# Performance work log

Hardware: AMD Instinct MI355X
Metric: run time of the kernel (lower is better)

Reference implementation:

```python
import jax, jax.numpy as jnp
import numpy as np
import math

H = 16          # attn_heads
DK = 64         # features_dec // attn_heads
NEG = -1e9      # additive causal mask value
EPS = 1e-6      # LayerNorm eps (annotated transformer)


def get_slopes(n):
    def p2(m):
        start = 2.0 ** (-(2.0 ** (-(math.log2(m) - 3))))
        return [start * start ** i for i in range(m)]
    if math.log2(n).is_integer():
        return p2(n)
    cp = 2 ** math.floor(math.log2(n))
    return p2(cp) + get_slopes(2 * cp)[0::2][: n - cp]


def setup_inputs() -> dict:
    key = jax.random.key(0)
    ks = jax.random.split(key, 12)
    B, S, FT, FDZ, FDEC, FD = 8, 1024, 16, 768, 1024, 16

    def lin(k, out_d, in_d):
        return jax.random.normal(k, (out_d, in_d), jnp.float32) / np.float32(np.sqrt(in_d))

    return {
        "z_sample": jax.random.normal(ks[0], (B, FDZ), jnp.float32),
        "r_traj": jax.random.normal(ks[1], (B, S, FT), jnp.float32),
        "dense_w": lin(ks[2], FDEC, FDZ + FT), "dense_b": jnp.zeros((FDEC,), jnp.float32),
        "ln_g": jnp.ones((FDEC,), jnp.float32), "ln_b": jnp.zeros((FDEC,), jnp.float32),
        "wq": lin(ks[3], FDEC, FDEC), "bq": jnp.zeros((FDEC,), jnp.float32),
        "wk": lin(ks[4], FDEC, FDEC), "bk": jnp.zeros((FDEC,), jnp.float32),
        "wv": lin(ks[5], FDEC, FDEC), "bv": jnp.zeros((FDEC,), jnp.float32),
        "wo": lin(ks[6], FDEC, FDEC), "bo": jnp.zeros((FDEC,), jnp.float32),
        "dec_w": lin(ks[7], FD, FDEC), "dec_b": jnp.zeros((FD,), jnp.float32),
    }


def reference(z_sample, r_traj, dense_w, dense_b, ln_g, ln_b,
              wq, bq, wk, bk, wv, bv, wo, bo, dec_w, dec_b):
    B, S, _ = r_traj.shape
    # concat trajectory features with broadcast latent sample -> [B,S,in_size]
    x = jnp.concatenate(
        [r_traj, jnp.broadcast_to(z_sample[:, None, :], (B, S, z_sample.shape[-1]))], axis=-1)
    x = x @ dense_w.T + dense_b  # [B,S,FDEC]

    # causal additive mask + ALiBi bias: bias[h,i,j] = causal(i,j) + slope_h * j
    slopes = jnp.asarray(get_slopes(H), jnp.float32)
    causal = jnp.triu(jnp.full((S, S), NEG, jnp.float32), k=1)
    bias = causal[None, :, :] + slopes[:, None, None] * jnp.arange(S, dtype=jnp.float32)[None, None, :]  # [H,S,S]

    # pre-norm sublayer: x + attn(LN(x))  (dropout=0 / eval)
    mu = x.mean(-1, keepdims=True)
    var = x.var(-1, keepdims=True)
    xn = ln_g * (x - mu) / jnp.sqrt(var + EPS) + ln_b

    def heads(w, b):
        return (xn @ w.T + b).reshape(B, S, H, DK).transpose(0, 2, 1, 3)  # [B,H,S,DK]

    q, k, v = heads(wq, bq), heads(wk, bk), heads(wv, bv)
    scores = jnp.einsum('bhid,bhjd->bhij', q, k) / np.float32(np.sqrt(DK)) + bias[None]
    attn = jax.nn.softmax(scores, axis=-1)
    o = jnp.einsum('bhij,bhjd->bhid', attn, v).transpose(0, 2, 1, 3).reshape(B, S, H * DK)
    x = x + o @ wo.T + bo

    # decode_state then transpose(-2,-1) -> [B, features_d, S]
    return (x @ dec_w.T + dec_b).transpose(0, 2, 1)
```

## Files before the change

kernel.cpp:

```cpp
#include <hip/hip_runtime.h>

static constexpr int Bn   = 8;
static constexpr int S    = 1024;
static constexpr int FT   = 16;
static constexpr int FDZ  = 768;
static constexpr int INK  = 784;
static constexpr int FDEC = 1024;
static constexpr int M    = Bn * S;
static constexpr int H    = 16;
static constexpr int FD   = 16;

typedef __bf16 bf16x8 __attribute__((ext_vector_type(8)));
typedef float  f32x4  __attribute__((ext_vector_type(4)));

__device__ __forceinline__ unsigned short f2b(float f) {
  return __builtin_bit_cast(unsigned short, static_cast<__bf16>(f));
}
__device__ __forceinline__ float b2f(unsigned short u) {
  return (float)__builtin_bit_cast(__bf16, u);
}

__device__ __forceinline__ void gload16(const void* g, void* l) {
  __builtin_amdgcn_global_load_lds(
      (const __attribute__((address_space(1))) unsigned int*)g,
      (__attribute__((address_space(3))) unsigned int*)l, 16, 0, 0);
}

__global__ __launch_bounds__(256) void k_prep(const float* __restrict__ dnw,
                                              const float* __restrict__ wq,
                                              const float* __restrict__ wk,
                                              const float* __restrict__ wv,
                                              const float* __restrict__ dcw,
                                              const float* __restrict__ bq,
                                              const float* __restrict__ bk,
                                              const float* __restrict__ bv,
                                              unsigned short* __restrict__ w3,
                                              unsigned short* __restrict__ dwb,
                                              float* __restrict__ b3,
                                              unsigned short* __restrict__ wt16) {
  const int bid = blockIdx.x, tid = threadIdx.x;
  const int c = tid * 4;
  if (bid < 3072) {
    const int r = bid;
    const float* src = (r < 1024) ? wq : (r < 2048 ? wk : wv);
    const int rr = r & 1023;
    float4 v = *reinterpret_cast<const float4*>(&src[(size_t)rr * 1024 + c]);
    unsigned short o4[4] = {f2b(v.x), f2b(v.y), f2b(v.z), f2b(v.w)};
    *reinterpret_cast<uint2*>(&w3[(size_t)r * 1024 + c]) = *reinterpret_cast<uint2*>(o4);
  } else if (bid < 3088) {
    const int r = bid - 3072;
    float4 v = *reinterpret_cast<const float4*>(&dcw[(size_t)r * 1024 + c]);
    unsigned short o4[4] = {f2b(v.x), f2b(v.y), f2b(v.z), f2b(v.w)};
    *reinterpret_cast<uint2*>(&dwb[(size_t)r * 1024 + c]) = *reinterpret_cast<uint2*>(o4);
  } else if (bid < 3091) {
    const int r = bid - 3088;
    const float* s = (r == 0) ? bq : (r == 1 ? bk : bv);
    *reinterpret_cast<float4*>(&b3[r * 1024 + c]) =
        *reinterpret_cast<const float4*>(&s[c]);
  } else {
    const int idx = (bid - 3091) * 256 + tid;
    const int k = idx >> 10, cc = idx & 1023;
    wt16[k * 1024 + cc] = f2b(dnw[(size_t)cc * INK + k]);
  }
}

__global__ __launch_bounds__(256) void k_wcomb1(const float* __restrict__ dcw,
                                                const float* __restrict__ wo,
                                                const float* __restrict__ bo,
                                                const float* __restrict__ dcb,
                                                float* __restrict__ part,
                                                float* __restrict__ bias2) {
  const int tid = threadIdx.x;
  if (blockIdx.x < 64) {
    const int kb = blockIdx.x;
    const int c = tid * 4;
    const int k0 = kb * 16;
    float4 wv[16];
#pragma unroll
    for (int k = 0; k < 16; k++)
      wv[k] = *reinterpret_cast<const float4*>(&wo[(size_t)(k0 + k) * 1024 + c]);
#pragma unroll
    for (int i = 0; i < 16; i++) {
      float4 a = make_float4(0.f, 0.f, 0.f, 0.f);
#pragma unroll
      for (int k = 0; k < 16; k++) {
        float d = dcw[i * 1024 + k0 + k];
        a.x += d * wv[k].x; a.y += d * wv[k].y;
        a.z += d * wv[k].z; a.w += d * wv[k].w;
      }
      *reinterpret_cast<float4*>(&part[((size_t)kb * 16 + i) * 1024 + c]) = a;
    }
  } else {
    const int lane = tid & 63, w = tid >> 6;
    for (int q = 0; q < 4; q++) {
      int f = w * 4 + q;
      const float* dp = &dcw[(size_t)f * 1024];
      float s = 0.f;
#pragma unroll
      for (int t = 0; t < 16; t++) {
        int k = lane + t * 64;
        s += dp[k] * bo[k];
      }
      for (int off = 32; off; off >>= 1) s += __shfl_down(s, off);
      if (lane == 0) bias2[f] = s + dcb[f];
    }
  }
}

__global__ __launch_bounds__(256) void k_wcomb2(const float* __restrict__ part,
                                                unsigned short* __restrict__ wcombb) {
  const int idx = blockIdx.x * 256 + threadIdx.x;
  float s = 0.f;
#pragma unroll 8
  for (int kb = 0; kb < 64; kb++) s += part[(size_t)kb * 16384 + idx];
  wcombb[idx] = f2b(s);
}

__global__ __launch_bounds__(256) void k_za(const float* __restrict__ z,
                                            const float* __restrict__ dnw,
                                            float* __restrict__ za) {
  const int tid = threadIdx.x, lane = tid & 63, w = tid >> 6;
  const int idx = blockIdx.x * 4 + w;
  const int col = idx >> 3, b = idx & 7;
  const float* wp = &dnw[(size_t)col * INK + FT];
  const float* zp = &z[b * FDZ];
  float s = 0.f;
#pragma unroll
  for (int i = 0; i < 12; i++) {
    int k = lane + i * 64;
    s += wp[k] * zp[k];
  }
  for (int off = 32; off; off >>= 1) s += __shfl_down(s, off);
  if (lane == 0) za[b * 1024 + col] = s;
}

__global__ __launch_bounds__(256) void k_dense_ln(const float* __restrict__ rt,
                                                  const float* __restrict__ za,
                                                  const float* __restrict__ dnb,
                                                  const float* __restrict__ lng,
                                                  const float* __restrict__ lnb,
                                                  const unsigned short* __restrict__ wt16g,
                                                  unsigned short* __restrict__ xres,
                                                  unsigned short* __restrict__ xn) {
  __shared__ unsigned short wt[16 * 1024];
  __shared__ float ss[4], qq[4];
  const int tid = threadIdx.x, lane = tid & 63, wv = tid >> 6;
  const int c0 = tid * 4;
#pragma unroll
  for (int i = 0; i < 8; i++)
    reinterpret_cast<uint4*>(wt)[tid + 256 * i] =
        reinterpret_cast<const uint4*>(wt16g)[tid + 256 * i];
  const float4 bv  = *reinterpret_cast<const float4*>(&dnb[c0]);
  const float4 gv  = *reinterpret_cast<const float4*>(&lng[c0]);
  const float4 bev = *reinterpret_cast<const float4*>(&lnb[c0]);
  __syncthreads();

  for (int r = 0; r < 4; ++r) {
    const int m = blockIdx.x * 4 + r;
    const int b = m >> 10;
    float rtv[16];
    {
      float4 t0 = *reinterpret_cast<const float4*>(&rt[m * 16 + 0]);
      float4 t1 = *reinterpret_cast<const float4*>(&rt[m * 16 + 4]);
      float4 t2 = *reinterpret_cast<const float4*>(&rt[m * 16 + 8]);
      float4 t3 = *reinterpret_cast<const float4*>(&rt[m * 16 + 12]);
      rtv[0]=t0.x; rtv[1]=t0.y; rtv[2]=t0.z; rtv[3]=t0.w;
      rtv[4]=t1.x; rtv[5]=t1.y; rtv[6]=t1.z; rtv[7]=t1.w;
      rtv[8]=t2.x; rtv[9]=t2.y; rtv[10]=t2.z; rtv[11]=t2.w;
      rtv[12]=t3.x; rtv[13]=t3.y; rtv[14]=t3.z; rtv[15]=t3.w;
    }
    float4 zav = *reinterpret_cast<const float4*>(&za[b * 1024 + c0]);
    float acc[4] = {zav.x + bv.x, zav.y + bv.y, zav.z + bv.z, zav.w + bv.w};
#pragma unroll
    for (int k = 0; k < 16; ++k) {
      uint2 wraw = *reinterpret_cast<const uint2*>(&wt[k * 1024 + c0]);
      const unsigned short* wp = reinterpret_cast<const unsigned short*>(&wraw);
      float rk = rtv[k];
      acc[0] += rk * b2f(wp[0]);
      acc[1] += rk * b2f(wp[1]);
      acc[2] += rk * b2f(wp[2]);
      acc[3] += rk * b2f(wp[3]);
    }
    float s = acc[0] + acc[1] + acc[2] + acc[3];
    float q = acc[0]*acc[0] + acc[1]*acc[1] + acc[2]*acc[2] + acc[3]*acc[3];
    for (int off = 32; off; off >>= 1) { s += __shfl_down(s, off); q += __shfl_down(q, off); }
    if (lane == 0) { ss[wv] = s; qq[wv] = q; }
    __syncthreads();
    float St = ss[0] + ss[1] + ss[2] + ss[3];
    float Qt = qq[0] + qq[1] + qq[2] + qq[3];
    float mu  = St * (1.f / 1024.f);
    float var = Qt * (1.f / 1024.f) - mu * mu;
    float rstd = rsqrtf(var + 1e-6f);
    unsigned short xo[4], no[4];
    xo[0] = f2b(acc[0]); no[0] = f2b(gv.x * (acc[0] - mu) * rstd + bev.x);
    xo[1] = f2b(acc[1]); no[1] = f2b(gv.y * (acc[1] - mu) * rstd + bev.y);
    xo[2] = f2b(acc[2]); no[2] = f2b(gv.z * (acc[2] - mu) * rstd + bev.z);
    xo[3] = f2b(acc[3]); no[3] = f2b(gv.w * (acc[3] - mu) * rstd + bev.w);
    *reinterpret_cast<uint2*>(&xres[(size_t)m * 1024 + c0]) = *reinterpret_cast<uint2*>(xo);
    *reinterpret_cast<uint2*>(&xn[(size_t)m * 1024 + c0])   = *reinterpret_cast<uint2*>(no);
    __syncthreads();
  }
}

template<int EPI>
__global__ __launch_bounds__(256, 3) void k_gemm1(const unsigned short* __restrict__ A, int lda,
                                                  const unsigned short* __restrict__ Bw, int ldb,
                                                  int K, int N,
                                                  const float* __restrict__ bias,
                                                  unsigned short* __restrict__ Cb) {
  __shared__ __align__(16) unsigned short As[3 * 128 * 32];
  __shared__ __align__(16) unsigned short Bs[3 * 128 * 32];
  const int tid = threadIdx.x, lane = tid & 63, w = tid >> 6;
  const int wr = w >> 1, wc = w & 1;
  const int lr = lane & 15, lg = lane >> 4;

  const int xcd = blockIdx.x & 7;
  const int j   = blockIdx.x >> 3;
  const int m0  = (xcd * 8 + (j & 7)) * 128;
  const int n0  = (j >> 3) * 128;

  const int nt = K >> 5;

  const int g0 = tid;
  const int r0g = g0 >> 2, c0g = (g0 & 3) ^ ((r0g >> 1) & 3);
  const int g1 = tid + 256;
  const int r1g = g1 >> 2, c1g = (g1 & 3) ^ ((r1g >> 1) & 3);
  const unsigned short* srcA0 = A + (size_t)(m0 + r0g) * lda + c0g * 8;
  const unsigned short* srcA1 = A + (size_t)(m0 + r1g) * lda + c1g * 8;
  const unsigned short* srcB0 = Bw + (size_t)(n0 + r0g) * ldb + c0g * 8;
  const unsigned short* srcB1 = Bw + (size_t)(n0 + r1g) * ldb + c1g * 8;
  const int d0 = (w * 64) * 8;
  const int d1 = (256 + w * 64) * 8;

  int offA[4], offB[4];
#pragma unroll
  for (int mi = 0; mi < 4; mi++) {
    int r = wr * 64 + mi * 16 + lr;
    offA[mi] = r * 32 + (lg ^ ((r >> 1) & 3)) * 8;
  }
#pragma unroll
  for (int ni = 0; ni < 4; ni++) {
    int r = wc * 64 + ni * 16 + lr;
    offB[ni] = r * 32 + (lg ^ ((r >> 1) & 3)) * 8;
  }

  f32x4 acc[4][4];
#pragma unroll
  for (int i = 0; i < 4; i++)
#pragma unroll
    for (int j2 = 0; j2 < 4; j2++)
#pragma unroll
      for (int e = 0; e < 4; e++) acc[i][j2][e] = 0.f;

  auto stage = [&](int tt) {
    const int sl = tt % 3;
    const size_t ko = (size_t)tt * 32;
    gload16(srcA0 + ko, &As[sl * 4096 + d0]);
    gload16(srcA1 + ko, &As[sl * 4096 + d1]);
    gload16(srcB0 + ko, &Bs[sl * 4096 + d0]);
    gload16(srcB1 + ko, &Bs[sl * 4096 + d1]);
  };
  auto compute = [&](int tt) {
    const int sl = (tt % 3) * 4096;
    bf16x8 af[4], bfr[4];
#pragma unroll
    for (int mi = 0; mi < 4; mi++)
      af[mi] = *reinterpret_cast<const bf16x8*>(&As[sl + offA[mi]]);
#pragma unroll
    for (int ni = 0; ni < 4; ni++)
      bfr[ni] = *reinterpret_cast<const bf16x8*>(&Bs[sl + offB[ni]]);
    __builtin_amdgcn_s_setprio(1);
#pragma unroll
    for (int mi = 0; mi < 4; mi++)
#pragma unroll
      for (int ni = 0; ni < 4; ni++)
        acc[mi][ni] = __builtin_amdgcn_mfma_f32_16x16x32_bf16(af[mi], bfr[ni], acc[mi][ni], 0, 0, 0);
    __builtin_amdgcn_s_setprio(0);
  };

  stage(0); stage(1);

  int t = 0;
  for (; t < nt - 2; ++t) {
    asm volatile("s_waitcnt vmcnt(4)" ::: "memory");
    __builtin_amdgcn_s_barrier();
    stage(t + 2);
    compute(t);
  }
  asm volatile("s_waitcnt vmcnt(4)" ::: "memory");
  __builtin_amdgcn_s_barrier();
  compute(t); ++t;
  asm volatile("s_waitcnt vmcnt(0)" ::: "memory");
  __builtin_amdgcn_s_barrier();
  compute(t);

#pragma unroll
  for (int mi = 0; mi < 4; mi++)
#pragma unroll
    for (int ni = 0; ni < 4; ni++) {
      int col = n0 + wc * 64 + ni * 16 + lr;
      float bv = bias ? bias[col] : 0.f;
#pragma unroll
      for (int jj = 0; jj < 4; jj++) {
        int row = m0 + wr * 64 + mi * 16 + lg * 4 + jj;
        float v = acc[mi][ni][jj] + bv;
        Cb[(size_t)row * N + col] = f2b(v);
      }
    }
}

__global__ __launch_bounds__(512, 4) void k_attn(const unsigned short* __restrict__ qkv,
                                                 unsigned short* __restrict__ o) {
  __shared__ unsigned short Ks[2][64][72];
  __shared__ unsigned short Vt[2][64][72];
  __shared__ unsigned short Pl[8][16][72];
  const int tid = threadIdx.x, lane = tid & 63, w = tid >> 6;
  const int bh = blockIdx.x, b = bh >> 4, h = bh & 15;
  const int lr = lane & 15, lg = lane >> 4, lg4 = lg * 4;
  const int krow = tid >> 3, c8 = (tid & 7) << 3;
  const int kb8 = krow >> 3, kl = krow & 7, vq = tid & 7;
  const float slope2 = exp2f(-0.5f * (float)(h + 1)) * 1.44269504f;
  const float sc2 = 0.125f * 1.44269504f;

  for (int ph = 0; ph < 2; ++ph) {
    const int qb = ph ? (7 - (int)blockIdx.y) : (int)blockIdx.y;
    const int q0 = qb * 128;
    const int qlo = q0 + w * 16;
    const int qa = qlo + lr;

    bf16x8 qf0, qf1;
    {
      const unsigned short* qp = &qkv[(size_t)(b * 1024 + qlo + lr) * 3072 + h * 64];
      qf0 = *reinterpret_cast<const bf16x8*>(qp + lg * 8);
      qf1 = *reinterpret_cast<const bf16x8*>(qp + 32 + lg * 8);
    }
    float mrun = -3.0e38f, lrun = 0.f;
    f32x4 accO[4];
    for (int dn = 0; dn < 4; dn++)
      for (int e = 0; e < 4; e++) accO[dn][e] = 0.f;

    const int nt = 2 * qb + 2;
    uint4 kr, vr;
    {
      const size_t base = (size_t)(b * 1024 + krow) * 3072 + h * 64;
      kr = *reinterpret_cast<const uint4*>(&qkv[base + 1024 + c8]);
      vr = *reinterpret_cast<const uint4*>(&qkv[base + 2048 + c8]);
    }
    *reinterpret_cast<uint4*>(&Ks[0][krow][c8]) = kr;
    {
      const unsigned short* vs = reinterpret_cast<const unsigned short*>(&vr);
      for (int jj = 0; jj < 8; jj++)
        Vt[0][c8 + jj][((kb8 ^ vq) << 3) | kl] = vs[jj];
    }
    __syncthreads();

    for (int kt = 0; kt < nt; ++kt) {
      const int kb = kt << 6;
      const int cb = kt & 1, nb = cb ^ 1;
      const bool hn = (kt + 1 < nt);
      if (hn) {
        const size_t base = (size_t)(b * 1024 + kb + 64 + krow) * 3072 + h * 64;
        kr = *reinterpret_cast<const uint4*>(&qkv[base + 1024 + c8]);
        vr = *reinterpret_cast<const uint4*>(&qkv[base + 2048 + c8]);
      }
      const bool act = (kb <= qlo + 15);
      float f = 1.f;
      if (act) {
        f32x4 sf[4];
        for (int kn = 0; kn < 4; kn++) {
          f32x4 zz;
          for (int e = 0; e < 4; e++) zz[e] = 0.f;
          bf16x8 kf0 = *reinterpret_cast<const bf16x8*>(&Ks[cb][kn * 16 + lr][lg * 8]);
          bf16x8 kf1 = *reinterpret_cast<const bf16x8*>(&Ks[cb][kn * 16 + lr][32 + lg * 8]);
          zz = __builtin_amdgcn_mfma_f32_16x16x32_bf16(kf0, qf0, zz, 0, 0, 0);
          zz = __builtin_amdgcn_mfma_f32_16x16x32_bf16(kf1, qf1, zz, 0, 0, 0);
          sf[kn] = zz;
        }
        const bool needmask = (kb + 63 > qlo);
        float sc[4][4];
        float ml = -3.0e38f;
        for (int kn = 0; kn < 4; kn++) {
          float alib = slope2 * (float)(kb + kn * 16 + lg4);
          for (int jj = 0; jj < 4; jj++) {
            float v = fmaf(sf[kn][jj], sc2, alib + slope2 * (float)jj);
            if (needmask && (kb + kn * 16 + lg4 + jj > qa)) v = -3.0e38f;
            sc[kn][jj] = v;
            ml = fmaxf(ml, v);
          }
        }
        ml = fmaxf(ml, __shfl_xor(ml, 16));
        ml = fmaxf(ml, __shfl_xor(ml, 32));
        float mnew = fmaxf(mrun, ml);
        f = exp2f(mrun - mnew);
        float rs = 0.f;
        for (int kn = 0; kn < 4; kn++) {
          __bf16 pb[4];
          for (int jj = 0; jj < 4; jj++) {
            float pv = exp2f(sc[kn][jj] - mnew);
            rs += pv;
            pb[jj] = (__bf16)pv;
          }
          *reinterpret_cast<uint2*>(&Pl[w][lr][kn * 16 + lg4]) =
              *reinterpret_cast<uint2*>(pb);
        }
        rs += __shfl_xor(rs, 16);
        rs += __shfl_xor(rs, 32);
        lrun = lrun * f + rs;
        mrun = mnew;
      }
      if (hn) {
        *reinterpret_cast<uint4*>(&Ks[nb][krow][c8]) = kr;
        const unsigned short* vs = reinterpret_cast<const unsigned short*>(&vr);
        for (int jj = 0; jj < 8; jj++)
          Vt[nb][c8 + jj][((kb8 ^ vq) << 3) | kl] = vs[jj];
      }
      if (act) {
        float fj[4];
        for (int jj = 0; jj < 4; jj++) fj[jj] = __shfl(f, (lane & 48) | (lg4 + jj));
        for (int dn = 0; dn < 4; dn++)
          for (int jj = 0; jj < 4; jj++) accO[dn][jj] *= fj[jj];
        asm volatile("s_waitcnt lgkmcnt(0)" ::: "memory");
        for (int ks = 0; ks < 2; ks++) {
          bf16x8 pa = *reinterpret_cast<const bf16x8*>(&Pl[w][lr][ks * 32 + lg * 8]);
          for (int dn = 0; dn < 4; dn++) {
            int d = dn * 16 + lr;
            bf16x8 vb = *reinterpret_cast<const bf16x8*>(
                &Vt[cb][d][(((ks * 4 + lg) ^ (d >> 3)) << 3)]);
            accO[dn] = __builtin_amdgcn_mfma_f32_16x16x32_bf16(pa, vb, accO[dn], 0, 0, 0);
          }
        }
      }
      __syncthreads();
    }
    float linv[4];
    for (int jj = 0; jj < 4; jj++)
      linv[jj] = 1.f / __shfl(lrun, (lane & 48) | (lg4 + jj));
    for (int dn = 0; dn < 4; dn++)
      for (int jj = 0; jj < 4; jj++) {
        int row = qlo + lg4 + jj;
        int d = dn * 16 + lr;
        o[(size_t)(b * 1024 + row) * 1024 + h * 64 + d] = f2b(accO[dn][jj] * linv[jj]);
      }
  }
}

__global__ __launch_bounds__(256) void k_dec2(const unsigned short* __restrict__ xres,
                                              const unsigned short* __restrict__ ob,
                                              const unsigned short* __restrict__ dwb,
                                              const unsigned short* __restrict__ wcombb,
                                              const float* __restrict__ bias2,
                                              float* __restrict__ out) {
  const int tid = threadIdx.x, lane = tid & 63, w = tid >> 6;
  const int lr = lane & 15, lg = lane >> 4;
  const int sb = blockIdx.x * 4 + w;
  const int r0 = sb * 16;
  f32x4 acc;
  for (int e = 0; e < 4; e++) acc[e] = 0.f;
  const unsigned short* arow1 = &xres[(size_t)(r0 + lr) * 1024];
  const unsigned short* arow2 = &ob[(size_t)(r0 + lr) * 1024];
  const unsigned short* brow1 = &dwb[(size_t)lr * 1024];
  const unsigned short* brow2 = &wcombb[(size_t)lr * 1024];
  for (int k0 = 0; k0 < 1024; k0 += 32) {
    bf16x8 a1 = *reinterpret_cast<const bf16x8*>(arow1 + k0 + lg * 8);
    bf16x8 b1 = *reinterpret_cast<const bf16x8*>(brow1 + k0 + lg * 8);
    acc = __builtin_amdgcn_mfma_f32_16x16x32_bf16(a1, b1, acc, 0, 0, 0);
    bf16x8 a2 = *reinterpret_cast<const bf16x8*>(arow2 + k0 + lg * 8);
    bf16x8 b2 = *reinterpret_cast<const bf16x8*>(brow2 + k0 + lg * 8);
    acc = __builtin_amdgcn_mfma_f32_16x16x32_bf16(a2, b2, acc, 0, 0, 0);
  }
  const int b = r0 >> 10;
  const int sl = (r0 & 1023) + lg * 4;
  float bias = bias2[lr];
  float4 res;
  res.x = acc[0] + bias; res.y = acc[1] + bias; res.z = acc[2] + bias; res.w = acc[3] + bias;
  *reinterpret_cast<float4*>(&out[(size_t)(b * 16 + lr) * 1024 + sl]) = res;
}

extern "C" void kernel_launch(void* const* d_in, const int* in_sizes, int n_in,
                              void* d_out, int out_size, void* d_ws, size_t ws_size,
                              hipStream_t stream) {
  (void)in_sizes; (void)n_in; (void)out_size;
  const float* z   = (const float*)d_in[0];
  const float* rt  = (const float*)d_in[1];
  const float* dnw = (const float*)d_in[2];
  const float* dnb = (const float*)d_in[3];
  const float* lng = (const float*)d_in[4];
  const float* lnb = (const float*)d_in[5];
  const float* wq  = (const float*)d_in[6];
  const float* bq  = (const float*)d_in[7];
  const float* wk  = (const float*)d_in[8];
  const float* bk  = (const float*)d_in[9];
  const float* wv  = (const float*)d_in[10];
  const float* bv  = (const float*)d_in[11];
  const float* wo  = (const float*)d_in[12];
  const float* bo  = (const float*)d_in[13];
  const float* dcw = (const float*)d_in[14];
  const float* dcb = (const float*)d_in[15];
  float* out = (float*)d_out;

  char* p = (char*)d_ws;
  unsigned short* xres  = (unsigned short*)p; p += (size_t)M * FDEC * 2;
  unsigned short* xn    = (unsigned short*)p; p += (size_t)M * FDEC * 2;
  unsigned short* w3    = (unsigned short*)p; p += (size_t)3 * FDEC * FDEC * 2;
  float* b3             = (float*)p;          p += (size_t)3 * FDEC * 4;
  unsigned short* qkv   = (unsigned short*)p; p += (size_t)M * 3 * FDEC * 2;
  unsigned short* ob    = (unsigned short*)p; p += (size_t)M * FDEC * 2;
  unsigned short* dwb   = (unsigned short*)p; p += (size_t)FD * FDEC * 2;
  unsigned short* wcombb= (unsigned short*)p; p += (size_t)FD * FDEC * 2;
  float* bias2          = (float*)p;          p += (size_t)FD * 4;
  float* za             = (float*)p;          p += (size_t)8 * 1024 * 4;
  unsigned short* wt16  = (unsigned short*)p; p += (size_t)16 * 1024 * 2;
  float* part           = (float*)p;          p += (size_t)64 * FD * FDEC * 4;
  if ((size_t)(p - (char*)d_ws) > ws_size) return;

  k_prep<<<3155, 256, 0, stream>>>(dnw, wq, wk, wv, dcw, bq, bk, bv,
                                   w3, dwb, b3, wt16);
  k_wcomb1<<<65, 256, 0, stream>>>(dcw, wo, bo, dcb, part, bias2);
  k_wcomb2<<<64, 256, 0, stream>>>(part, wcombb);
  k_za<<<2048, 256, 0, stream>>>(z, dnw, za);
  k_dense_ln<<<2048, 256, 0, stream>>>(rt, za, dnb, lng, lnb, wt16, xres, xn);
  k_gemm1<1><<<(M / 128) * (3 * FDEC / 128), 256, 0, stream>>>(xn, FDEC, w3, FDEC, FDEC, 3 * FDEC, b3, qkv);
  k_attn<<<dim3(Bn * H, 4), 512, 0, stream>>>(qkv, ob);
  k_dec2<<<M / 64, 256, 0, stream>>>(xres, ob, dwb, wcombb, bias2, out);
}
```

Baseline: 168.3 us.

## Merge prep kernels and process paired causal query blocks in one K/V sweep

Result: faster. 159.9 us (-5.0%).

```diff
diff --git a/kernel.cpp b/kernel.cpp
--- a/kernel.cpp
+++ b/kernel.cpp
@@ -26,18 +26,25 @@
       (__attribute__((address_space(3))) unsigned int*)l, 16, 0, 0);
 }
 
-__global__ __launch_bounds__(256) void k_prep(const float* __restrict__ dnw,
-                                              const float* __restrict__ wq,
-                                              const float* __restrict__ wk,
-                                              const float* __restrict__ wv,
-                                              const float* __restrict__ dcw,
-                                              const float* __restrict__ bq,
-                                              const float* __restrict__ bk,
-                                              const float* __restrict__ bv,
-                                              unsigned short* __restrict__ w3,
-                                              unsigned short* __restrict__ dwb,
-                                              float* __restrict__ b3,
-                                              unsigned short* __restrict__ wt16) {
+__global__ __launch_bounds__(256) void k_pre(const float* __restrict__ dnw,
+                                             const float* __restrict__ wq,
+                                             const float* __restrict__ wk,
+                                             const float* __restrict__ wv,
+                                             const float* __restrict__ wo,
+                                             const float* __restrict__ dcw,
+                                             const float* __restrict__ bq,
+                                             const float* __restrict__ bk,
+                                             const float* __restrict__ bv,
+                                             const float* __restrict__ bo,
+                                             const float* __restrict__ dcb,
+                                             const float* __restrict__ z,
+                                             unsigned short* __restrict__ w3,
+                                             unsigned short* __restrict__ dwb,
+                                             float* __restrict__ b3,
+                                             unsigned short* __restrict__ wt16,
+                                             float* __restrict__ part,
+                                             float* __restrict__ bias2,
+                                             float* __restrict__ za) {
   const int bid = blockIdx.x, tid = threadIdx.x;
   const int c = tid * 4;
   if (bid < 3072) {
@@ -57,40 +64,29 @@
     const float* s = (r == 0) ? bq : (r == 1 ? bk : bv);
     *reinterpret_cast<float4*>(&b3[r * 1024 + c]) =
         *reinterpret_cast<const float4*>(&s[c]);
-  } else {
+  } else if (bid < 3155) {
     const int idx = (bid - 3091) * 256 + tid;
     const int k = idx >> 10, cc = idx & 1023;
     wt16[k * 1024 + cc] = f2b(dnw[(size_t)cc * INK + k]);
-  }
-}
-
-__global__ __launch_bounds__(256) void k_wcomb1(const float* __restrict__ dcw,
-                                                const float* __restrict__ wo,
-                                                const float* __restrict__ bo,
-                                                const float* __restrict__ dcb,
-                                                float* __restrict__ part,
-                                                float* __restrict__ bias2) {
-  const int tid = threadIdx.x;
-  if (blockIdx.x < 64) {
-    const int kb = blockIdx.x;
-    const int c = tid * 4;
+  } else if (bid < 3219) {
+    const int kb = bid - 3155;
     const int k0 = kb * 16;
-    float4 wv[16];
+    float4 wv4[16];
 #pragma unroll
     for (int k = 0; k < 16; k++)
-      wv[k] = *reinterpret_cast<const float4*>(&wo[(size_t)(k0 + k) * 1024 + c]);
+      wv4[k] = *reinterpret_cast<const float4*>(&wo[(size_t)(k0 + k) * 1024 + c]);
 #pragma unroll
     for (int i = 0; i < 16; i++) {
       float4 a = make_float4(0.f, 0.f, 0.f, 0.f);
 #pragma unroll
       for (int k = 0; k < 16; k++) {
         float d = dcw[i * 1024 + k0 + k];
-        a.x += d * wv[k].x; a.y += d * wv[k].y;
-        a.z += d * wv[k].z; a.w += d * wv[k].w;
+        a.x += d * wv4[k].x; a.y += d * wv4[k].y;
+        a.z += d * wv4[k].z; a.w += d * wv4[k].w;
       }
       *reinterpret_cast<float4*>(&part[((size_t)kb * 16 + i) * 1024 + c]) = a;
     }
-  } else {
+  } else if (bid < 3220) {
     const int lane = tid & 63, w = tid >> 6;
     for (int q = 0; q < 4; q++) {
       int f = w * 4 + q;
@@ -104,47 +100,45 @@
       for (int off = 32; off; off >>= 1) s += __shfl_down(s, off);
       if (lane == 0) bias2[f] = s + dcb[f];
     }
-  }
-}
-
-__global__ __launch_bounds__(256) void k_wcomb2(const float* __restrict__ part,
-                                                unsigned short* __restrict__ wcombb) {
-  const int idx = blockIdx.x * 256 + threadIdx.x;
-  float s = 0.f;
+  } else {
+    const int lane = tid & 63, w = tid >> 6;
+    const int idx = (bid - 3220) * 4 + w;
+    const int col = idx >> 3, b = idx & 7;
+    const float* wp = &dnw[(size_t)col * INK + FT];
+    const float* zp = &z[b * FDZ];
+    float s = 0.f;
+#pragma unroll
+    for (int i = 0; i < 12; i++) {
+      int k = lane + i * 64;
+      s += wp[k] * zp[k];
+    }
+    for (int off = 32; off; off >>= 1) s += __shfl_down(s, off);
+    if (lane == 0) za[b * 1024 + col] = s;
+  }
+}
+
+__global__ __launch_bounds__(256) void k_dln(const float* __restrict__ rt,
+                                             const float* __restrict__ za,
+                                             const float* __restrict__ dnb,
+                                             const float* __restrict__ lng,
+                                             const float* __restrict__ lnb,
+                                             const unsigned short* __restrict__ wt16g,
+                                             const float* __restrict__ part,
+                                             unsigned short* __restrict__ xres,
+                                             unsigned short* __restrict__ xn,
+                                             unsigned short* __restrict__ wcombb) {
+  const int tid = threadIdx.x;
+  if (blockIdx.x >= 2048) {
+    const int idx = (blockIdx.x - 2048) * 256 + tid;
+    float s = 0.f;
 #pragma unroll 8
-  for (int kb = 0; kb < 64; kb++) s += part[(size_t)kb * 16384 + idx];
-  wcombb[idx] = f2b(s);
-}
-
-__global__ __launch_bounds__(256) void k_za(const float* __restrict__ z,
-                                            const float* __restrict__ dnw,
-                                            float* __restrict__ za) {
-  const int tid = threadIdx.x, lane = tid & 63, w = tid >> 6;
-  const int idx = blockIdx.x * 4 + w;
-  const int col = idx >> 3, b = idx & 7;
-  const float* wp = &dnw[(size_t)col * INK + FT];
-  const float* zp = &z[b * FDZ];
-  float s = 0.f;
-#pragma unroll
-  for (int i = 0; i < 12; i++) {
-    int k = lane + i * 64;
-    s += wp[k] * zp[k];
-  }
-  for (int off = 32; off; off >>= 1) s += __shfl_down(s, off);
-  if (lane == 0) za[b * 1024 + col] = s;
-}
-
-__global__ __launch_bounds__(256) void k_dense_ln(const float* __restrict__ rt,
-                                                  const float* __restrict__ za,
-                                                  const float* __restrict__ dnb,
-                                                  const float* __restrict__ lng,
-                                                  const float* __restrict__ lnb,
-                                                  const unsigned short* __restrict__ wt16g,
-                                                  unsigned short* __restrict__ xres,
-                                                  unsigned short* __restrict__ xn) {
+    for (int kb = 0; kb < 64; kb++) s += part[(size_t)kb * 16384 + idx];
+    wcombb[idx] = f2b(s);
+    return;
+  }
   __shared__ unsigned short wt[16 * 1024];
   __shared__ float ss[4], qq[4];
-  const int tid = threadIdx.x, lane = tid & 63, wv = tid >> 6;
+  const int lane = tid & 63, wv = tid >> 6;
   const int c0 = tid * 4;
 #pragma unroll
   for (int i = 0; i < 8; i++)
@@ -322,126 +316,135 @@
   const float slope2 = exp2f(-0.5f * (float)(h + 1)) * 1.44269504f;
   const float sc2 = 0.125f * 1.44269504f;
 
-  for (int ph = 0; ph < 2; ++ph) {
-    const int qb = ph ? (7 - (int)blockIdx.y) : (int)blockIdx.y;
-    const int q0 = qb * 128;
-    const int qlo = q0 + w * 16;
-    const int qa = qlo + lr;
-
-    bf16x8 qf0, qf1;
-    {
-      const unsigned short* qp = &qkv[(size_t)(b * 1024 + qlo + lr) * 3072 + h * 64];
-      qf0 = *reinterpret_cast<const bf16x8*>(qp + lg * 8);
-      qf1 = *reinterpret_cast<const bf16x8*>(qp + 32 + lg * 8);
-    }
-    float mrun = -3.0e38f, lrun = 0.f;
-    f32x4 accO[4];
+  const int y = blockIdx.y;
+  const int qloA = y * 128 + w * 16;
+  const int qloB = (7 - y) * 128 + w * 16;
+  const int qaA = qloA + lr, qaB = qloB + lr;
+
+  bf16x8 qfA0, qfA1, qfB0, qfB1;
+  {
+    const unsigned short* qp = &qkv[(size_t)(b * 1024 + qloA + lr) * 3072 + h * 64];
+    qfA0 = *reinterpret_cast<const bf16x8*>(qp + lg * 8);
+    qfA1 = *reinterpret_cast<const bf16x8*>(qp + 32 + lg * 8);
+    const unsigned short* qp2 = &qkv[(size_t)(b * 1024 + qloB + lr) * 3072 + h * 64];
+    qfB0 = *reinterpret_cast<const bf16x8*>(qp2 + lg * 8);
+    qfB1 = *reinterpret_cast<const bf16x8*>(qp2 + 32 + lg * 8);
+  }
+  float mrunA = -3.0e38f, lrunA = 0.f, mrunB = -3.0e38f, lrunB = 0.f;
+  f32x4 accOA[4], accOB[4];
+  for (int dn = 0; dn < 4; dn++)
+    for (int e = 0; e < 4; e++) { accOA[dn][e] = 0.f; accOB[dn][e] = 0.f; }
+
+  const int nt = 16 - 2 * y;
+
+  auto proc = [&](int kb, int cb, int qlo, int qa, float& mrun, float& lrun,
+                  f32x4 (&accO)[4], bf16x8 qf0, bf16x8 qf1) {
+    f32x4 sf[4];
+    for (int kn = 0; kn < 4; kn++) {
+      f32x4 zz;
+      for (int e = 0; e < 4; e++) zz[e] = 0.f;
+      bf16x8 kf0 = *reinterpret_cast<const bf16x8*>(&Ks[cb][kn * 16 + lr][lg * 8]);
+      bf16x8 kf1 = *reinterpret_cast<const bf16x8*>(&Ks[cb][kn * 16 + lr][32 + lg * 8]);
+      zz = __builtin_amdgcn_mfma_f32_16x16x32_bf16(kf0, qf0, zz, 0, 0, 0);
+      zz = __builtin_amdgcn_mfma_f32_16x16x32_bf16(kf1, qf1, zz, 0, 0, 0);
+      sf[kn] = zz;
+    }
+    const bool needmask = (kb + 63 > qlo);
+    float sc[4][4];
+    float ml = -3.0e38f;
+    for (int kn = 0; kn < 4; kn++) {
+      float alib = slope2 * (float)(kb + kn * 16 + lg4);
+      for (int jj = 0; jj < 4; jj++) {
+        float v = fmaf(sf[kn][jj], sc2, alib + slope2 * (float)jj);
+        if (needmask && (kb + kn * 16 + lg4 + jj > qa)) v = -3.0e38f;
+        sc[kn][jj] = v;
+        ml = fmaxf(ml, v);
+      }
+    }
+    ml = fmaxf(ml, __shfl_xor(ml, 16));
+    ml = fmaxf(ml, __shfl_xor(ml, 32));
+    float mnew = fmaxf(mrun, ml);
+    float f = exp2f(mrun - mnew);
+    float rs = 0.f;
+    for (int kn = 0; kn < 4; kn++) {
+      __bf16 pb[4];
+      for (int jj = 0; jj < 4; jj++) {
+        float pv = exp2f(sc[kn][jj] - mnew);
+        rs += pv;
+        pb[jj] = (__bf16)pv;
+      }
+      *reinterpret_cast<uint2*>(&Pl[w][lr][kn * 16 + lg4]) =
+          *reinterpret_cast<uint2*>(pb);
+    }
+    rs += __shfl_xor(rs, 16);
+    rs += __shfl_xor(rs, 32);
+    lrun = lrun * f + rs;
+    mrun = mnew;
+    float fj[4];
+    for (int jj = 0; jj < 4; jj++) fj[jj] = __shfl(f, (lane & 48) | (lg4 + jj));
     for (int dn = 0; dn < 4; dn++)
-      for (int e = 0; e < 4; e++) accO[dn][e] = 0.f;
-
-    const int nt = 2 * qb + 2;
-    uint4 kr, vr;
-    {
-      const size_t base = (size_t)(b * 1024 + krow) * 3072 + h * 64;
+      for (int jj = 0; jj < 4; jj++) accO[dn][jj] *= fj[jj];
+    asm volatile("s_waitcnt lgkmcnt(0)" ::: "memory");
+    for (int ks = 0; ks < 2; ks++) {
+      bf16x8 pa = *reinterpret_cast<const bf16x8*>(&Pl[w][lr][ks * 32 + lg * 8]);
+      for (int dn = 0; dn < 4; dn++) {
+        int d = dn * 16 + lr;
+        bf16x8 vb = *reinterpret_cast<const bf16x8*>(
+            &Vt[cb][d][(((ks * 4 + lg) ^ (d >> 3)) << 3)]);
+        accO[dn] = __builtin_amdgcn_mfma_f32_16x16x32_bf16(pa, vb, accO[dn], 0, 0, 0);
+      }
+    }
+  };
+
+  uint4 kr, vr;
+  {
+    const size_t base = (size_t)(b * 1024 + krow) * 3072 + h * 64;
+    kr = *reinterpret_cast<const uint4*>(&qkv[base + 1024 + c8]);
+    vr = *reinterpret_cast<const uint4*>(&qkv[base + 2048 + c8]);
+  }
+  *reinterpret_cast<uint4*>(&Ks[0][krow][c8]) = kr;
+  {
+    const unsigned short* vs = reinterpret_cast<const unsigned short*>(&vr);
+    for (int jj = 0; jj < 8; jj++)
+      Vt[0][c8 + jj][((kb8 ^ vq) << 3) | kl] = vs[jj];
+  }
+  __syncthreads();
+
+  for (int kt = 0; kt < nt; ++kt) {
+    const int kb = kt << 6;
+    const int cb = kt & 1, nb = cb ^ 1;
+    const bool hn = (kt + 1 < nt);
+    if (hn) {
+      const size_t base = (size_t)(b * 1024 + kb + 64 + krow) * 3072 + h * 64;
       kr = *reinterpret_cast<const uint4*>(&qkv[base + 1024 + c8]);
       vr = *reinterpret_cast<const uint4*>(&qkv[base + 2048 + c8]);
     }
-    *reinterpret_cast<uint4*>(&Ks[0][krow][c8]) = kr;
-    {
+    if (kb <= qloA + 15)
+      proc(kb, cb, qloA, qaA, mrunA, lrunA, accOA, qfA0, qfA1);
+    if (hn) {
+      *reinterpret_cast<uint4*>(&Ks[nb][krow][c8]) = kr;
       const unsigned short* vs = reinterpret_cast<const unsigned short*>(&vr);
       for (int jj = 0; jj < 8; jj++)
-        Vt[0][c8 + jj][((kb8 ^ vq) << 3) | kl] = vs[jj];
-    }
+        Vt[nb][c8 + jj][((kb8 ^ vq) << 3) | kl] = vs[jj];
+    }
+    if (kb <= qloB + 15)
+      proc(kb, cb, qloB, qaB, mrunB, lrunB, accOB, qfB0, qfB1);
     __syncthreads();
-
-    for (int kt = 0; kt < nt; ++kt) {
-      const int kb = kt << 6;
-      const int cb = kt & 1, nb = cb ^ 1;
-      const bool hn = (kt + 1 < nt);
-      if (hn) {
-        const size_t base = (size_t)(b * 1024 + kb + 64 + krow) * 3072 + h * 64;
-        kr = *reinterpret_cast<const uint4*>(&qkv[base + 1024 + c8]);
-        vr = *reinterpret_cast<const uint4*>(&qkv[base + 2048 + c8]);
-      }
-      const bool act = (kb <= qlo + 15);
-      float f = 1.f;
-      if (act) {
-        f32x4 sf[4];
-        for (int kn = 0; kn < 4; kn++) {
-          f32x4 zz;
-          for (int e = 0; e < 4; e++) zz[e] = 0.f;
-          bf16x8 kf0 = *reinterpret_cast<const bf16x8*>(&Ks[cb][kn * 16 + lr][lg * 8]);
-          bf16x8 kf1 = *reinterpret_cast<const bf16x8*>(&Ks[cb][kn * 16 + lr][32 + lg * 8]);
-          zz = __builtin_amdgcn_mfma_f32_16x16x32_bf16(kf0, qf0, zz, 0, 0, 0);
-          zz = __builtin_amdgcn_mfma_f32_16x16x32_bf16(kf1, qf1, zz, 0, 0, 0);
-          sf[kn] = zz;
-        }
-        const bool needmask = (kb + 63 > qlo);
-        float sc[4][4];
-        float ml = -3.0e38f;
-        for (int kn = 0; kn < 4; kn++) {
-          float alib = slope2 * (float)(kb + kn * 16 + lg4);
-          for (int jj = 0; jj < 4; jj++) {
-            float v = fmaf(sf[kn][jj], sc2, alib + slope2 * (float)jj);
-            if (needmask && (kb + kn * 16 + lg4 + jj > qa)) v = -3.0e38f;
-            sc[kn][jj] = v;
-            ml = fmaxf(ml, v);
-          }
-        }
-        ml = fmaxf(ml, __shfl_xor(ml, 16));
-        ml = fmaxf(ml, __shfl_xor(ml, 32));
-        float mnew = fmaxf(mrun, ml);
-        f = exp2f(mrun - mnew);
-        float rs = 0.f;
-        for (int kn = 0; kn < 4; kn++) {
-          __bf16 pb[4];
-          for (int jj = 0; jj < 4; jj++) {
-            float pv = exp2f(sc[kn][jj] - mnew);
-            rs += pv;
-            pb[jj] = (__bf16)pv;
-          }
-          *reinterpret_cast<uint2*>(&Pl[w][lr][kn * 16 + lg4]) =
-              *reinterpret_cast<uint2*>(pb);
-        }
-        rs += __shfl_xor(rs, 16);
-        rs += __shfl_xor(rs, 32);
-        lrun = lrun * f + rs;
-        mrun = mnew;
-      }
-      if (hn) {
-        *reinterpret_cast<uint4*>(&Ks[nb][krow][c8]) = kr;
-        const unsigned short* vs = reinterpret_cast<const unsigned short*>(&vr);
-        for (int jj = 0; jj < 8; jj++)
-          Vt[nb][c8 + jj][((kb8 ^ vq) << 3) | kl] = vs[jj];
-      }
-      if (act) {
-        float fj[4];
-        for (int jj = 0; jj < 4; jj++) fj[jj] = __shfl(f, (lane & 48) | (lg4 + jj));
-        for (int dn = 0; dn < 4; dn++)
-          for (int jj = 0; jj < 4; jj++) accO[dn][jj] *= fj[jj];
-        asm volatile("s_waitcnt lgkmcnt(0)" ::: "memory");
-        for (int ks = 0; ks < 2; ks++) {
-          bf16x8 pa = *reinterpret_cast<const bf16x8*>(&Pl[w][lr][ks * 32 + lg * 8]);
-          for (int dn = 0; dn < 4; dn++) {
-            int d = dn * 16 + lr;
-            bf16x8 vb = *reinterpret_cast<const bf16x8*>(
-                &Vt[cb][d][(((ks * 4 + lg) ^ (d >> 3)) << 3)]);
-            accO[dn] = __builtin_amdgcn_mfma_f32_16x16x32_bf16(pa, vb, accO[dn], 0, 0, 0);
-          }
-        }
-      }
-      __syncthreads();
-    }
-    float linv[4];
-    for (int jj = 0; jj < 4; jj++)
-      linv[jj] = 1.f / __shfl(lrun, (lane & 48) | (lg4 + jj));
-    for (int dn = 0; dn < 4; dn++)
-      for (int jj = 0; jj < 4; jj++) {
-        int row = qlo + lg4 + jj;
-        int d = dn * 16 + lr;
-        o[(size_t)(b * 1024 + row) * 1024 + h * 64 + d] = f2b(accO[dn][jj] * linv[jj]);
-      }
-  }
+  }
+
+  float linvA[4], linvB[4];
+  for (int jj = 0; jj < 4; jj++) {
+    linvA[jj] = 1.f / __shfl(lrunA, (lane & 48) | (lg4 + jj));
+    linvB[jj] = 1.f / __shfl(lrunB, (lane & 48) | (lg4 + jj));
+  }
+  for (int dn = 0; dn < 4; dn++)
+    for (int jj = 0; jj < 4; jj++) {
+      int d = dn * 16 + lr;
+      int rowA = qloA + lg4 + jj;
+      o[(size_t)(b * 1024 + rowA) * 1024 + h * 64 + d] = f2b(accOA[dn][jj] * linvA[jj]);
+      int rowB = qloB + lg4 + jj;
+      o[(size_t)(b * 1024 + rowB) * 1024 + h * 64 + d] = f2b(accOB[dn][jj] * linvB[jj]);
+    }
 }
 
 __global__ __launch_bounds__(256) void k_dec2(const unsigned short* __restrict__ xres,
@@ -513,12 +516,9 @@
   float* part           = (float*)p;          p += (size_t)64 * FD * FDEC * 4;
   if ((size_t)(p - (char*)d_ws) > ws_size) return;
 
-  k_prep<<<3155, 256, 0, stream>>>(dnw, wq, wk, wv, dcw, bq, bk, bv,
-                                   w3, dwb, b3, wt16);
-  k_wcomb1<<<65, 256, 0, stream>>>(dcw, wo, bo, dcb, part, bias2);
-  k_wcomb2<<<64, 256, 0, stream>>>(part, wcombb);
-  k_za<<<2048, 256, 0, stream>>>(z, dnw, za);
-  k_dense_ln<<<2048, 256, 0, stream>>>(rt, za, dnb, lng, lnb, wt16, xres, xn);
+  k_pre<<<5268, 256, 0, stream>>>(dnw, wq, wk, wv, wo, dcw, bq, bk, bv, bo, dcb, z,
+                                  w3, dwb, b3, wt16, part, bias2, za);
+  k_dln<<<2112, 256, 0, stream>>>(rt, za, dnb, lng, lnb, wt16, part, xres, xn, wcombb);
   k_gemm1<1><<<(M / 128) * (3 * FDEC / 128), 256, 0, stream>>>(xn, FDEC, w3, FDEC, FDEC, 3 * FDEC, b3, qkv);
   k_attn<<<dim3(Bn * H, 4), 512, 0, stream>>>(qkv, ob);
   k_dec2<<<M / 64, 256, 0, stream>>>(xres, ob, dwb, wcombb, bias2, out);
```
